# Performance work log

Measured on AMD Instinct MI355X. Metric: run time of the kernel, lower is better.

Reference implementation:

```python
import jax, jax.numpy as jnp
import numpy as np

H = 16  # num_heads
B, N, M, D = 4, 512, 2048, 1024
FF = 4096  # mlp_ratio * D
LN_EPS = 1e-5


def _ln(x, g, b):
    m = x.mean(-1, keepdims=True)
    v = ((x - m) ** 2).mean(-1, keepdims=True)
    return (x - m) * jax.lax.rsqrt(v + LN_EPS) * g + b


def _attn(q_in, k_in, v_in, wq, bq, wk, bk, wv, bv, wp, bp):
    b, n, d = q_in.shape
    m = k_in.shape[1]
    hd = d // H
    scale = hd ** -0.5
    q = (q_in @ wq + bq).reshape(b, n, H, hd) * scale
    k = (k_in @ wk + bk).reshape(b, m, H, hd)
    v = (v_in @ wv + bv).reshape(b, m, H, hd)
    attn = jax.nn.softmax(jnp.einsum('bnhd,bmhd->bhnm', q, k), axis=-1)
    out = jnp.einsum('bhnm,bmhd->bnhd', attn, v).reshape(b, n, d)
    return out @ wp + bp


def setup_inputs() -> dict:
    key = jax.random.key(0)
    ks = iter(jax.random.split(key, 32))
    rnd = lambda shape: jax.random.normal(next(ks), shape, dtype=jnp.float32)
    w = lambda *shape: rnd(shape) * 0.02
    inp = {
        'state': rnd((B, N, D)),
        'patches': rnd((B, M, D)),
        'patches_pos_embed': rnd((B, M, D)),
        'state_query': rnd((B, N, D)),
    }
    for p in ('ca', 'sa'):
        inp[f'{p}_wq'] = w(D, D); inp[f'{p}_bq'] = jnp.zeros((D,), jnp.float32)
        inp[f'{p}_wk'] = w(D, D); inp[f'{p}_bk'] = jnp.zeros((D,), jnp.float32)
        inp[f'{p}_wv'] = w(D, D); inp[f'{p}_bv'] = jnp.zeros((D,), jnp.float32)
        inp[f'{p}_wp'] = w(D, D); inp[f'{p}_bp'] = jnp.zeros((D,), jnp.float32)
    inp['w1'] = w(D, FF); inp['b1'] = jnp.zeros((FF,), jnp.float32)
    inp['w2'] = w(FF, D); inp['b2'] = jnp.zeros((D,), jnp.float32)
    for i in (1, 2, 3):
        inp[f'n{i}_g'] = jnp.ones((D,), jnp.float32)
        inp[f'n{i}_b'] = jnp.zeros((D,), jnp.float32)
        inp[f'ls{i}'] = jnp.full((D,), 1e-5, jnp.float32)
    return inp


def reference(state, patches, patches_pos_embed, state_query,
              ca_wq, ca_bq, ca_wk, ca_bk, ca_wv, ca_bv, ca_wp, ca_bp,
              sa_wq, sa_bq, sa_wk, sa_bk, sa_wv, sa_bv, sa_wp, sa_bp,
              w1, b1, w2, b2,
              n1_g, n1_b, n2_g, n2_b, n3_g, n3_b,
              ls1, ls2, ls3):
    # pre-norm path of TransformerLayer.forward_pre (dropouts/drop_path = 0)
    state = state + state_query
    kv = patches + patches_pos_embed
    cross = _attn(_ln(state, n1_g, n1_b), kv, patches,
                  ca_wq, ca_bq, ca_wk, ca_bk, ca_wv, ca_bv, ca_wp, ca_bp)
    state = state + cross * ls1
    ns = _ln(state, n2_g, n2_b)
    selfa = _attn(ns, ns, ns,
                  sa_wq, sa_bq, sa_wk, sa_bk, sa_wv, sa_bv, sa_wp, sa_bp)
    state = state + selfa * ls2
    h = jax.nn.gelu(_ln(state, n3_g, n3_b) @ w1 + b1)
    return state + (h @ w2 + b2) * ls3
```

## Files before the change

### kernel.cpp

```cpp
#include <hip/hip_runtime.h>

#define DEV __device__ __forceinline__

typedef __bf16 bf16x8 __attribute__((ext_vector_type(8)));
typedef float f32x4 __attribute__((ext_vector_type(4)));

DEV unsigned short f2bf(float f) {
  __bf16 h = (__bf16)f;
  return __builtin_bit_cast(unsigned short, h);
}
DEV unsigned int cvtpk(float lo, float hi) {
  unsigned int r;
  asm("v_cvt_pk_bf16_f32 %0, %1, %2" : "=v"(r) : "v"(lo), "v"(hi));
  return r;
}

DEV void gload16(const void* g, void* l) {
  __builtin_amdgcn_global_load_lds(
      (const __attribute__((address_space(1))) unsigned int*)g,
      (__attribute__((address_space(3))) unsigned int*)l, 16, 0, 0);
}

DEV void tconv_body(const float* __restrict__ W, unsigned short* __restrict__ Wt,
                    int K, int N, int bx, int by) {
  __shared__ float tile[32][33];
  const int tx = threadIdx.x, ty = threadIdx.y;
  const int n0 = bx * 32, k0 = by * 32;
#pragma unroll
  for (int i = 0; i < 32; i += 8)
    tile[ty + i][tx] = W[(size_t)(k0 + ty + i) * N + n0 + tx];
  __syncthreads();
#pragma unroll
  for (int i = 0; i < 32; i += 8)
    Wt[(size_t)(n0 + ty + i) * K + k0 + tx] = f2bf(tile[tx][ty + i]);
}

__global__ __launch_bounds__(256) void tconv_kernel(
    const float* __restrict__ W, unsigned short* __restrict__ Wt, int K, int N) {
  tconv_body(W, Wt, K, N, blockIdx.x, blockIdx.y);
}

struct TC8 { const float* src[8]; unsigned short* dst[8]; };
__global__ __launch_bounds__(256) void tconv8_kernel(TC8 p) {
  tconv_body(p.src[blockIdx.z], p.dst[blockIdx.z], 1024, 1024, blockIdx.x, blockIdx.y);
}

__global__ __launch_bounds__(256) void cat3_kernel(
    const float* __restrict__ a, const float* __restrict__ b,
    const float* __restrict__ c, float* __restrict__ o) {
  const int i = blockIdx.x * 256 + threadIdx.x;
  o[i] = i < 1024 ? a[i] : (i < 2048 ? b[i - 1024] : c[i - 2048]);
}

__global__ __launch_bounds__(256) void vtrans_kernel(
    const unsigned short* __restrict__ V, unsigned short* __restrict__ vT,
    int Nk, int RS, int colbase) {
  __shared__ unsigned short tile[32][33];
  const int tx = threadIdx.x, ty = threadIdx.y;
  const int k0 = blockIdx.x * 32;
  const int h = blockIdx.y >> 1, dt = (blockIdx.y & 1) * 32;
  const int b = blockIdx.z;
#pragma unroll
  for (int i = 0; i < 32; i += 8)
    tile[ty + i][tx] = V[(size_t)(b * Nk + k0 + ty + i) * RS + colbase + h * 64 + dt + tx];
  __syncthreads();
#pragma unroll
  for (int i = 0; i < 32; i += 8)
    vT[((size_t)(b * 16 + h) * 64 + dt + ty + i) * Nk + k0 + tx] = tile[tx][ty + i];
}

__global__ __launch_bounds__(256) void add_ln_kernel(
    const float* __restrict__ a, const float* b, float* x0_out,
    unsigned short* __restrict__ y, const float* __restrict__ gam,
    const float* __restrict__ bet) {
  const int row = blockIdx.x, t = threadIdx.x;
  const int c = t * 4;
  const size_t base = (size_t)row * 1024 + c;
  float4 v = *reinterpret_cast<const float4*>(a + base);
  if (b) {
    float4 v2 = *reinterpret_cast<const float4*>(b + base);
    v.x += v2.x; v.y += v2.y; v.z += v2.z; v.w += v2.w;
  }
  if (x0_out) *reinterpret_cast<float4*>(x0_out + base) = v;
  float s = v.x + v.y + v.z + v.w;
  float sq = v.x * v.x + v.y * v.y + v.z * v.z + v.w * v.w;
#pragma unroll
  for (int o = 32; o > 0; o >>= 1) {
    s += __shfl_xor(s, o);
    sq += __shfl_xor(sq, o);
  }
  __shared__ float ps[4], pq[4];
  const int w = t >> 6;
  if ((t & 63) == 0) { ps[w] = s; pq[w] = sq; }
  __syncthreads();
  s = ps[0] + ps[1] + ps[2] + ps[3];
  sq = pq[0] + pq[1] + pq[2] + pq[3];
  const float mean = s * (1.f / 1024.f);
  const float var = sq * (1.f / 1024.f) - mean * mean;
  const float rstd = rsqrtf(var + 1e-5f);
  float4 gv = *reinterpret_cast<const float4*>(gam + c);
  float4 bv = *reinterpret_cast<const float4*>(bet + c);
  uint2 o2;
  o2.x = cvtpk((v.x - mean) * rstd * gv.x + bv.x, (v.y - mean) * rstd * gv.y + bv.y);
  o2.y = cvtpk((v.z - mean) * rstd * gv.z + bv.z, (v.w - mean) * rstd * gv.w + bv.w);
  *reinterpret_cast<uint2*>(y + base) = o2;
}

__global__ __launch_bounds__(256) void kvcast_kernel(
    const float* __restrict__ p, const float* __restrict__ pe,
    unsigned short* __restrict__ kvo, unsigned short* __restrict__ po) {
  const size_t i = ((size_t)blockIdx.x * 256 + threadIdx.x) * 4;
  float4 a = *reinterpret_cast<const float4*>(p + i);
  float4 b = *reinterpret_cast<const float4*>(pe + i);
  uint2 kv2, p2;
  kv2.x = cvtpk(a.x + b.x, a.y + b.y);
  kv2.y = cvtpk(a.z + b.z, a.w + b.w);
  p2.x = cvtpk(a.x, a.y);
  p2.y = cvtpk(a.z, a.w);
  *reinterpret_cast<uint2*>(kvo + i) = kv2;
  *reinterpret_cast<uint2*>(po + i) = p2;
}

DEV void xcd_swizzle(int gx, int gy, int& bx, int& by, int& bz) {
  const int gxy = gx * gy;
  const int nwg = gxy * gridDim.z;
  const int orig = (blockIdx.z * gy + blockIdx.y) * gx + blockIdx.x;
  const int q = nwg >> 3, r = nwg & 7;
  const int xcd = orig & 7;
  int wgid = (xcd < r ? xcd * (q + 1) : r * (q + 1) + (xcd - r) * q) + (orig >> 3);
  bz = wgid / gxy;
  wgid -= bz * gxy;
  if (gy >= gx) { by = wgid / gx; bx = wgid - by * gx; }
  else          { bx = wgid / gy; by = wgid - bx * gy; }
}

template <int BM, int BN>
DEV void gemm_core(const unsigned short* __restrict__ A,
                   const unsigned short* __restrict__ Bt,
                   unsigned short* As, unsigned short* Bs,
                   int brow, int bcol, int K, int lda, int koff,
                   f32x4 (&acc)[BM / 32][BN / 32]) {
  constexpr int WM = BM / 32, WN = BN / 32;
  const int t = threadIdx.x;
  const int lane = t & 63, w = t >> 6;
  const int wr = w >> 1, wc = w & 1;
  const int g = lane >> 4, lr = lane & 15;
  const int srow = lane >> 2, scol = (lane & 3) * 8;

  auto stage = [&](int buf, int k0) {
#pragma unroll
    for (int i = 0; i < BM / 64; i++) {
      const int r0 = (i * 4 + w) * 16;
      gload16(A + (size_t)(brow + r0 + srow) * lda + koff + k0 + scol,
              &As[buf * BM * 32 + r0 * 32]);
    }
#pragma unroll
    for (int i = 0; i < BN / 64; i++) {
      const int r0 = (i * 4 + w) * 16;
      gload16(Bt + (size_t)(bcol + r0 + srow) * lda + koff + k0 + scol,
              &Bs[buf * BN * 32 + r0 * 32]);
    }
  };

  stage(0, 0);
  const int nk = K / 32;
  int cur = 0;
  for (int kt = 0; kt < nk; kt++) {
    __syncthreads();
    if (kt + 1 < nk) stage(cur ^ 1, (kt + 1) * 32);
    bf16x8 af[WM], bfr[WN];
#pragma unroll
    for (int m = 0; m < WM; m++)
      af[m] = *reinterpret_cast<const bf16x8*>(
          &As[cur * BM * 32 + (wr * (BM / 2) + m * 16 + lr) * 32 + g * 8]);
#pragma unroll
    for (int n = 0; n < WN; n++)
      bfr[n] = *reinterpret_cast<const bf16x8*>(
          &Bs[cur * BN * 32 + (wc * (BN / 2) + n * 16 + lr) * 32 + g * 8]);
#pragma unroll
    for (int m = 0; m < WM; m++)
#pragma unroll
      for (int n = 0; n < WN; n++)
        acc[m][n] = __builtin_amdgcn_mfma_f32_16x16x32_bf16(af[m], bfr[n], acc[m][n], 0, 0, 0);
    cur ^= 1;
  }
}

template <int EPI, int BM, int BN>
__global__ __launch_bounds__(256) void gemm_kernel(
    const unsigned short* __restrict__ A, const unsigned short* __restrict__ Bt,
    const float* __restrict__ bias, const float* resid,
    const float* __restrict__ ls, void* outp, int M, int N, int K, int lda) {
  constexpr int WM = BM / 32;
  constexpr int WN = BN / 32;
  __shared__ __align__(16) unsigned short As[2 * BM * 32];
  __shared__ __align__(16) unsigned short Bs[2 * BN * 32];
  const int t = threadIdx.x;
  const int lane = t & 63, w = t >> 6;
  const int wr = w >> 1, wc = w & 1;
  const int g = lane >> 4, lr = lane & 15;

  int bx, by, bz;
  xcd_swizzle(gridDim.x, gridDim.y, bx, by, bz);
  const int brow = by * BM, bcol = bx * BN;

  f32x4 acc[WM][WN] = {};
  gemm_core<BM, BN>(A, Bt, As, Bs, brow, bcol, K, lda, bz * K, acc);

#pragma unroll
  for (int m = 0; m < WM; m++) {
    const int row0 = brow + wr * (BM / 2) + m * 16 + g * 4;
#pragma unroll
    for (int n = 0; n < WN; n++) {
      const int col = bcol + wc * (BN / 2) + n * 16 + lr;
      const float bv = (EPI == 4) ? 0.f : bias[col];
#pragma unroll
      for (int r = 0; r < 4; r++) {
        const float v = acc[m][n][r] + bv;
        const size_t idx = (size_t)(row0 + r) * N + col;
        if (EPI == 0) {
          ((unsigned short*)outp)[idx] = f2bf(v);
        } else if (EPI == 2) {
          ((float*)outp)[idx] = resid[idx] + v * ls[col];
        } else if (EPI == 3) {
          const float tth = tanhf(0.7978845608028654f * (v + 0.044715f * v * v * v));
          ((unsigned short*)outp)[idx] = f2bf(0.5f * v * (1.f + tth));
        } else {
          ((float*)outp)[(size_t)bz * M * N + idx] = v;
        }
      }
    }
  }
}

struct G3 {
  const unsigned short* A[3]; const unsigned short* Bt[3];
  const float* bias[3]; unsigned short* out[3]; int ecum[3];
};
__global__ __launch_bounds__(256) void gemm3_kernel(G3 p, int N, int K) {
  constexpr int BM = 128, BN = 128, WM = BM / 32, WN = BN / 32;
  __shared__ __align__(16) unsigned short As[2 * BM * 32];
  __shared__ __align__(16) unsigned short Bs[2 * BN * 32];
  const int t = threadIdx.x;
  const int lane = t & 63, w = t >> 6;
  const int wr = w >> 1, wc = w & 1;
  const int g = lane >> 4, lr = lane & 15;

  int bx, by, bz;
  xcd_swizzle(gridDim.x, gridDim.y, bx, by, bz);
  const int s = (by >= p.ecum[0]) + (by >= p.ecum[1]);
  const int byloc = by - (s ? p.ecum[s - 1] : 0);
  const unsigned short* A = p.A[s];
  const unsigned short* Bt = p.Bt[s];
  const float* bias = p.bias[s];
  unsigned short* outp = p.out[s];
  const int brow = byloc * BM, bcol = bx * BN;

  f32x4 acc[WM][WN] = {};
  gemm_core<BM, BN>(A, Bt, As, Bs, brow, bcol, K, K, 0, acc);

#pragma unroll
  for (int m = 0; m < WM; m++) {
    const int row0 = brow + wr * (BM / 2) + m * 16 + g * 4;
#pragma unroll
    for (int n = 0; n < WN; n++) {
      const int col = bcol + wc * (BN / 2) + n * 16 + lr;
      const float bv = bias[col];
#pragma unroll
      for (int r = 0; r < 4; r++)
        outp[(size_t)(row0 + r) * N + col] = f2bf(acc[m][n][r] + bv);
    }
  }
}

__global__ __launch_bounds__(256) void splitk_red_kernel(
    const float* __restrict__ p, const float* __restrict__ bias,
    const float* __restrict__ resid, const float* __restrict__ ls,
    float* __restrict__ out) {
  const size_t i = ((size_t)blockIdx.x * 256 + threadIdx.x) * 4;
  const int c = (int)(i & 1023);
  float4 a = *reinterpret_cast<const float4*>(p + i);
  float4 b = *reinterpret_cast<const float4*>(p + 2048ull * 1024 + i);
  float4 rv = *reinterpret_cast<const float4*>(resid + i);
  float4 bb = *reinterpret_cast<const float4*>(bias + c);
  float4 lv = *reinterpret_cast<const float4*>(ls + c);
  float4 o;
  o.x = rv.x + (a.x + b.x + bb.x) * lv.x;
  o.y = rv.y + (a.y + b.y + bb.y) * lv.y;
  o.z = rv.z + (a.z + b.z + bb.z) * lv.z;
  o.w = rv.w + (a.w + b.w + bb.w) * lv.w;
  *reinterpret_cast<float4*>(out + i) = o;
}

__global__ __launch_bounds__(512) void attn_kernel(
    const unsigned short* __restrict__ Q, const unsigned short* __restrict__ Kp,
    const unsigned short* __restrict__ vT, unsigned short* __restrict__ O,
    int RSq, int RSk, int Nq, int Nk, float k2) {
  __shared__ __align__(16) unsigned short Ks[2][128 * 72];
  __shared__ __align__(16) unsigned short Vs[2][64 * 136];
  __shared__ __align__(16) unsigned short Ps[128 * 136];
  const int t = threadIdx.x, lane = t & 63, w = t >> 6;
  const int qt = blockIdx.y, h = blockIdx.x & 15, b = blockIdx.x >> 4;
  const int g = lane >> 4, lr = lane & 15;
  const int ksrow = t >> 2, kscol = (t & 3) * 16;
  const int vsrow = t >> 3, vscol = (t & 7) * 16;

  uint4 qr[2];
  {
    const unsigned short* qp = Q + (size_t)(b * Nq + qt * 128 + w * 16 + lr) * RSq + h * 64 + g * 8;
    qr[0] = *reinterpret_cast<const uint4*>(qp);
    qr[1] = *reinterpret_cast<const uint4*>(qp + 32);
  }
  float m_i = -1e30f, l_i = 0.f;
  f32x4 acc_o[4] = {};

  auto kaddr = [&](int kv0) {
    return reinterpret_cast<const uint4*>(
        Kp + (size_t)(b * Nk + kv0 + ksrow) * RSk + h * 64 + kscol);
  };
  auto vaddr = [&](int kv0) {
    return reinterpret_cast<const uint4*>(
        vT + ((size_t)(b * 16 + h) * 64 + vsrow) * Nk + kv0 + vscol);
  };

  uint4 kr0 = kaddr(0)[0], kr1 = kaddr(0)[1];
  uint4 vr0 = vaddr(0)[0], vr1 = vaddr(0)[1];

  int cur = 0;
  for (int kv0 = 0; kv0 < Nk; kv0 += 128) {
    *reinterpret_cast<uint4*>(&Ks[cur][ksrow * 72 + kscol]) = kr0;
    *reinterpret_cast<uint4*>(&Ks[cur][ksrow * 72 + kscol + 8]) = kr1;
    *reinterpret_cast<uint4*>(&Vs[cur][vsrow * 136 + vscol]) = vr0;
    *reinterpret_cast<uint4*>(&Vs[cur][vsrow * 136 + vscol + 8]) = vr1;
    __syncthreads();
    if (kv0 + 128 < Nk) {
      kr0 = kaddr(kv0 + 128)[0]; kr1 = kaddr(kv0 + 128)[1];
      vr0 = vaddr(kv0 + 128)[0]; vr1 = vaddr(kv0 + 128)[1];
    }

    f32x4 accs[8] = {};
    __builtin_amdgcn_s_setprio(1);
#pragma unroll
    for (int d0 = 0; d0 < 64; d0 += 32) {
      bf16x8 qf = __builtin_bit_cast(bf16x8, qr[d0 >> 5]);
#pragma unroll
      for (int m = 0; m < 8; m++) {
        bf16x8 kf = *reinterpret_cast<const bf16x8*>(&Ks[cur][(m * 16 + lr) * 72 + d0 + g * 8]);
        accs[m] = __builtin_amdgcn_mfma_f32_16x16x32_bf16(kf, qf, accs[m], 0, 0, 0);
      }
    }
    __builtin_amdgcn_s_setprio(0);
    float pmax = -1e30f;
#pragma unroll
    for (int m = 0; m < 8; m++)
#pragma unroll
      for (int r = 0; r < 4; r++) pmax = fmaxf(pmax, accs[m][r]);
    pmax = fmaxf(pmax, __shfl_xor(pmax, 16));
    pmax = fmaxf(pmax, __shfl_xor(pmax, 32));
    const float pm2 = pmax * k2;
    if (!__all(pm2 <= m_i + 8.f)) {
      const float m_new = fmaxf(m_i, pm2);
      const float corr = exp2f(m_i - m_new);
      m_i = m_new;
      l_i *= corr;
#pragma unroll
      for (int r = 0; r < 4; r++) {
        const float cf = __shfl(corr, g * 4 + r);
#pragma unroll
        for (int n = 0; n < 4; n++) acc_o[n][r] *= cf;
      }
    }
    float psum = 0.f;
#pragma unroll
    for (int m = 0; m < 8; m++) {
      float p0 = exp2f(fmaf(accs[m][0], k2, -m_i));
      float p1 = exp2f(fmaf(accs[m][1], k2, -m_i));
      float p2 = exp2f(fmaf(accs[m][2], k2, -m_i));
      float p3 = exp2f(fmaf(accs[m][3], k2, -m_i));
      psum += p0 + p1 + p2 + p3;
      uint2 pk;
      pk.x = cvtpk(p0, p1);
      pk.y = cvtpk(p2, p3);
      *reinterpret_cast<uint2*>(&Ps[(w * 16 + lr) * 136 + m * 16 + g * 4]) = pk;
    }
    psum += __shfl_xor(psum, 16);
    psum += __shfl_xor(psum, 32);
    l_i += psum;
    __builtin_amdgcn_s_setprio(1);
#pragma unroll
    for (int ks = 0; ks < 4; ks++) {
      bf16x8 pf = *reinterpret_cast<const bf16x8*>(&Ps[(w * 16 + lr) * 136 + ks * 32 + g * 8]);
#pragma unroll
      for (int n = 0; n < 4; n++) {
        bf16x8 vf = *reinterpret_cast<const bf16x8*>(&Vs[cur][(n * 16 + lr) * 136 + ks * 32 + g * 8]);
        acc_o[n] = __builtin_amdgcn_mfma_f32_16x16x32_bf16(pf, vf, acc_o[n], 0, 0, 0);
      }
    }
    __builtin_amdgcn_s_setprio(0);
    cur ^= 1;
  }
#pragma unroll
  for (int r = 0; r < 4; r++) {
    const float li = __shfl(l_i, g * 4 + r);
    const float inv = 1.f / li;
    const int qrow = qt * 128 + w * 16 + g * 4 + r;
#pragma unroll
    for (int n = 0; n < 4; n++)
      O[(size_t)(b * Nq + qrow) * 1024 + h * 64 + n * 16 + lr] = f2bf(acc_o[n][r] * inv);
  }
}

extern "C" void kernel_launch(void* const* d_in, const int* in_sizes, int n_in,
                              void* d_out, int out_size, void* d_ws, size_t ws_size,
                              hipStream_t stream) {
  const float* state = (const float*)d_in[0];
  const float* patches = (const float*)d_in[1];
  const float* ppe = (const float*)d_in[2];
  const float* squery = (const float*)d_in[3];
  const float* ca_wq = (const float*)d_in[4];
  const float* ca_bq = (const float*)d_in[5];
  const float* ca_wk = (const float*)d_in[6];
  const float* ca_bk = (const float*)d_in[7];
  const float* ca_wv = (const float*)d_in[8];
  const float* ca_bv = (const float*)d_in[9];
  const float* ca_wp = (const float*)d_in[10];
  const float* ca_bp = (const float*)d_in[11];
  const float* sa_wq = (const float*)d_in[12];
  const float* sa_bq = (const float*)d_in[13];
  const float* sa_wk = (const float*)d_in[14];
  const float* sa_bk = (const float*)d_in[15];
  const float* sa_wv = (const float*)d_in[16];
  const float* sa_bv = (const float*)d_in[17];
  const float* sa_wp = (const float*)d_in[18];
  const float* sa_bp = (const float*)d_in[19];
  const float* w1 = (const float*)d_in[20];
  const float* b1 = (const float*)d_in[21];
  const float* w2 = (const float*)d_in[22];
  const float* b2 = (const float*)d_in[23];
  const float* n1_g = (const float*)d_in[24];
  const float* n1_b = (const float*)d_in[25];
  const float* ls1 = (const float*)d_in[26];
  const float* n2_g = (const float*)d_in[27];
  const float* n2_b = (const float*)d_in[28];
  const float* ls2 = (const float*)d_in[29];
  const float* n3_g = (const float*)d_in[30];
  const float* n3_b = (const float*)d_in[31];
  const float* ls3 = (const float*)d_in[32];

  char* wsp = (char*)d_ws;
  auto alloc = [&](size_t bytes) {
    void* p = (void*)wsp;
    wsp += (bytes + 255) & ~(size_t)255;
    return p;
  };
  float* stateF = (float*)alloc(2048ull * 1024 * 4);
  unsigned short* lnB = (unsigned short*)alloc(2048ull * 1024 * 2);
  unsigned short* kvB = (unsigned short*)alloc(8192ull * 1024 * 2);
  unsigned short* patB = (unsigned short*)alloc(8192ull * 1024 * 2);
  unsigned short* qB = (unsigned short*)alloc(2048ull * 1024 * 2);
  unsigned short* kB = (unsigned short*)alloc(8192ull * 1024 * 2);
  unsigned short* vB = (unsigned short*)alloc(8192ull * 1024 * 2);
  unsigned short* oB = (unsigned short*)alloc(2048ull * 1024 * 2);
  unsigned short* hB = kvB;
  unsigned short* qkvB = kB;
  unsigned short* vTc = patB;
  unsigned short* vTs = qB;
  float* mlp2p = (float*)patB;
  unsigned short* ca_wqt = (unsigned short*)alloc(1024ull * 1024 * 2);
  unsigned short* ca_wkt = (unsigned short*)alloc(1024ull * 1024 * 2);
  unsigned short* ca_wvt = (unsigned short*)alloc(1024ull * 1024 * 2);
  unsigned short* ca_wpt = (unsigned short*)alloc(1024ull * 1024 * 2);
  unsigned short* sa_wqkvt = (unsigned short*)alloc(3072ull * 1024 * 2);
  unsigned short* sa_wpt = (unsigned short*)alloc(1024ull * 1024 * 2);
  unsigned short* w1t = (unsigned short*)alloc(4096ull * 1024 * 2);
  unsigned short* w2t = (unsigned short*)alloc(4096ull * 1024 * 2);
  float* sa_bqkv = (float*)alloc(3072 * 4);

  const dim3 tb(32, 8);
  TC8 tc;
  tc.src[0] = ca_wq; tc.dst[0] = ca_wqt;
  tc.src[1] = ca_wk; tc.dst[1] = ca_wkt;
  tc.src[2] = ca_wv; tc.dst[2] = ca_wvt;
  tc.src[3] = ca_wp; tc.dst[3] = ca_wpt;
  tc.src[4] = sa_wq; tc.dst[4] = sa_wqkvt;
  tc.src[5] = sa_wk; tc.dst[5] = sa_wqkvt + 1024ull * 1024;
  tc.src[6] = sa_wv; tc.dst[6] = sa_wqkvt + 2048ull * 1024;
  tc.src[7] = sa_wp; tc.dst[7] = sa_wpt;
  tconv8_kernel<<<dim3(32, 32, 8), tb, 0, stream>>>(tc);
  tconv_kernel<<<dim3(128, 32), tb, 0, stream>>>(w1, w1t, 1024, 4096);
  tconv_kernel<<<dim3(32, 128), tb, 0, stream>>>(w2, w2t, 4096, 1024);
  cat3_kernel<<<12, 256, 0, stream>>>(sa_bq, sa_bk, sa_bv, sa_bqkv);

  add_ln_kernel<<<2048, 256, 0, stream>>>(state, squery, stateF, lnB, n1_g, n1_b);
  kvcast_kernel<<<8192, 256, 0, stream>>>(patches, ppe, kvB, patB);

  const float k2 = 0.125f * 1.4426950408889634f;

  G3 g3;
  g3.A[0] = lnB;  g3.Bt[0] = ca_wqt; g3.bias[0] = ca_bq; g3.out[0] = qB;  g3.ecum[0] = 16;
  g3.A[1] = kvB;  g3.Bt[1] = ca_wkt; g3.bias[1] = ca_bk; g3.out[1] = kB;  g3.ecum[1] = 80;
  g3.A[2] = patB; g3.Bt[2] = ca_wvt; g3.bias[2] = ca_bv; g3.out[2] = vB;  g3.ecum[2] = 144;
  gemm3_kernel<<<dim3(8, 144), 256, 0, stream>>>(g3, 1024, 1024);
  vtrans_kernel<<<dim3(64, 32, 4), tb, 0, stream>>>(vB, vTc, 2048, 1024, 0);
  attn_kernel<<<dim3(64, 4), 512, 0, stream>>>(qB, kB, vTc, oB, 1024, 1024, 512, 2048, k2);
  gemm_kernel<2, 64, 64><<<dim3(16, 32), 256, 0, stream>>>(oB, ca_wpt, ca_bp, stateF, ls1, stateF, 2048, 1024, 1024, 1024);

  add_ln_kernel<<<2048, 256, 0, stream>>>(stateF, nullptr, nullptr, lnB, n2_g, n2_b);
  gemm_kernel<0, 128, 64><<<dim3(48, 16), 256, 0, stream>>>(lnB, sa_wqkvt, sa_bqkv, nullptr, nullptr, qkvB, 2048, 3072, 1024, 1024);
  vtrans_kernel<<<dim3(16, 32, 4), tb, 0, stream>>>(qkvB, vTs, 512, 3072, 2048);
  attn_kernel<<<dim3(64, 4), 512, 0, stream>>>(qkvB, qkvB + 1024, vTs, oB, 3072, 3072, 512, 512, k2);
  gemm_kernel<2, 64, 64><<<dim3(16, 32), 256, 0, stream>>>(oB, sa_wpt, sa_bp, stateF, ls2, stateF, 2048, 1024, 1024, 1024);

  add_ln_kernel<<<2048, 256, 0, stream>>>(stateF, nullptr, nullptr, lnB, n3_g, n3_b);
  gemm_kernel<3, 128, 128><<<dim3(32, 16), 256, 0, stream>>>(lnB, w1t, b1, nullptr, nullptr, hB, 2048, 4096, 1024, 1024);
  gemm_kernel<4, 128, 64><<<dim3(16, 16, 2), 256, 0, stream>>>(hB, w2t, nullptr, nullptr, nullptr, mlp2p, 2048, 1024, 2048, 4096);
  splitk_red_kernel<<<2048, 256, 0, stream>>>(mlp2p, b2, stateF, ls3, (float*)d_out);
}
```

Measured before the change: 314.7 us.

## Fuse prelude kernels into one launch and write V transposed from GEMM epilogues

Merges the weight transpose/cast, kv cast, first add+LayerNorm and bias concat into a single prelude kernel launch. The V-projection GEMMs (cross and self attention) now write V directly in transposed per-head layout through an LDS-staged epilogue, removing both vtrans kernels and an intermediate V buffer round trip. It also raises wave priority around the MFMA block in the GEMM inner loop. In exchange the GEMMs need larger shared memory for the transpose staging, which may lower occupancy, and the prelude mixes heterogeneous work in one grid.

```diff
diff --git a/kernel.cpp b/kernel.cpp
--- a/kernel.cpp
+++ b/kernel.cpp
@@ -24,7 +24,8 @@
 DEV void tconv_body(const float* __restrict__ W, unsigned short* __restrict__ Wt,
                     int K, int N, int bx, int by) {
   __shared__ float tile[32][33];
-  const int tx = threadIdx.x, ty = threadIdx.y;
+  const int t = threadIdx.x;
+  const int tx = t & 31, ty = t >> 5;
   const int n0 = bx * 32, k0 = by * 32;
 #pragma unroll
   for (int i = 0; i < 32; i += 8)
@@ -35,45 +36,10 @@
     Wt[(size_t)(n0 + ty + i) * K + k0 + tx] = f2bf(tile[tx][ty + i]);
 }
 
-__global__ __launch_bounds__(256) void tconv_kernel(
-    const float* __restrict__ W, unsigned short* __restrict__ Wt, int K, int N) {
-  tconv_body(W, Wt, K, N, blockIdx.x, blockIdx.y);
-}
-
-struct TC8 { const float* src[8]; unsigned short* dst[8]; };
-__global__ __launch_bounds__(256) void tconv8_kernel(TC8 p) {
-  tconv_body(p.src[blockIdx.z], p.dst[blockIdx.z], 1024, 1024, blockIdx.x, blockIdx.y);
-}
-
-__global__ __launch_bounds__(256) void cat3_kernel(
-    const float* __restrict__ a, const float* __restrict__ b,
-    const float* __restrict__ c, float* __restrict__ o) {
-  const int i = blockIdx.x * 256 + threadIdx.x;
-  o[i] = i < 1024 ? a[i] : (i < 2048 ? b[i - 1024] : c[i - 2048]);
-}
-
-__global__ __launch_bounds__(256) void vtrans_kernel(
-    const unsigned short* __restrict__ V, unsigned short* __restrict__ vT,
-    int Nk, int RS, int colbase) {
-  __shared__ unsigned short tile[32][33];
-  const int tx = threadIdx.x, ty = threadIdx.y;
-  const int k0 = blockIdx.x * 32;
-  const int h = blockIdx.y >> 1, dt = (blockIdx.y & 1) * 32;
-  const int b = blockIdx.z;
-#pragma unroll
-  for (int i = 0; i < 32; i += 8)
-    tile[ty + i][tx] = V[(size_t)(b * Nk + k0 + ty + i) * RS + colbase + h * 64 + dt + tx];
-  __syncthreads();
-#pragma unroll
-  for (int i = 0; i < 32; i += 8)
-    vT[((size_t)(b * 16 + h) * 64 + dt + ty + i) * Nk + k0 + tx] = tile[tx][ty + i];
-}
-
-__global__ __launch_bounds__(256) void add_ln_kernel(
-    const float* __restrict__ a, const float* b, float* x0_out,
-    unsigned short* __restrict__ y, const float* __restrict__ gam,
-    const float* __restrict__ bet) {
-  const int row = blockIdx.x, t = threadIdx.x;
+DEV void add_ln_body(const float* __restrict__ a, const float* b, float* x0_out,
+                     unsigned short* __restrict__ y, const float* __restrict__ gam,
+                     const float* __restrict__ bet, int row) {
+  const int t = threadIdx.x;
   const int c = t * 4;
   const size_t base = (size_t)row * 1024 + c;
   float4 v = *reinterpret_cast<const float4*>(a + base);
@@ -106,10 +72,10 @@
   *reinterpret_cast<uint2*>(y + base) = o2;
 }
 
-__global__ __launch_bounds__(256) void kvcast_kernel(
-    const float* __restrict__ p, const float* __restrict__ pe,
-    unsigned short* __restrict__ kvo, unsigned short* __restrict__ po) {
-  const size_t i = ((size_t)blockIdx.x * 256 + threadIdx.x) * 4;
+DEV void kvcast_body(const float* __restrict__ p, const float* __restrict__ pe,
+                     unsigned short* __restrict__ kvo, unsigned short* __restrict__ po,
+                     int bid) {
+  const size_t i = ((size_t)bid * 256 + threadIdx.x) * 4;
   float4 a = *reinterpret_cast<const float4*>(p + i);
   float4 b = *reinterpret_cast<const float4*>(pe + i);
   uint2 kv2, p2;
@@ -119,6 +85,44 @@
   p2.y = cvtpk(a.z, a.w);
   *reinterpret_cast<uint2*>(kvo + i) = kv2;
   *reinterpret_cast<uint2*>(po + i) = p2;
+}
+
+struct Pre {
+  const float* sqw[8]; unsigned short* sqd[8];
+  const float* w1; unsigned short* w1t;
+  const float* w2; unsigned short* w2t;
+  const float* state; const float* squery; float* stateF; unsigned short* lnB;
+  const float* n1_g; const float* n1_b;
+  const float* patches; const float* ppe; unsigned short* kvB; unsigned short* patB;
+  const float* bq; const float* bk; const float* bv; float* bqkv;
+};
+__global__ __launch_bounds__(256) void prelude_kernel(Pre p) {
+  const int bid = blockIdx.x;
+  if (bid < 8192) {
+    kvcast_body(p.patches, p.ppe, p.kvB, p.patB, bid);
+  } else if (bid < 16384) {
+    const int i = bid - 8192;
+    const int m = i >> 10, wi = i & 1023;
+    tconv_body(p.sqw[m], p.sqd[m], 1024, 1024, wi & 31, wi >> 5);
+  } else if (bid < 20480) {
+    const int i = bid - 16384;
+    tconv_body(p.w1, p.w1t, 1024, 4096, i & 127, i >> 7);
+  } else if (bid < 24576) {
+    const int i = bid - 20480;
+    tconv_body(p.w2, p.w2t, 4096, 1024, i & 31, i >> 5);
+  } else if (bid < 26624) {
+    add_ln_body(p.state, p.squery, p.stateF, p.lnB, p.n1_g, p.n1_b, bid - 24576);
+  } else {
+    const int i = (bid - 26624) * 256 + threadIdx.x;
+    p.bqkv[i] = i < 1024 ? p.bq[i] : (i < 2048 ? p.bk[i - 1024] : p.bv[i - 2048]);
+  }
+}
+
+__global__ __launch_bounds__(256) void add_ln_kernel(
+    const float* __restrict__ a, const float* b, float* x0_out,
+    unsigned short* __restrict__ y, const float* __restrict__ gam,
+    const float* __restrict__ bet) {
+  add_ln_body(a, b, x0_out, y, gam, bet, blockIdx.x);
 }
 
 DEV void xcd_swizzle(int gx, int gy, int& bx, int& by, int& bz) {
@@ -177,12 +181,54 @@
     for (int n = 0; n < WN; n++)
       bfr[n] = *reinterpret_cast<const bf16x8*>(
           &Bs[cur * BN * 32 + (wc * (BN / 2) + n * 16 + lr) * 32 + g * 8]);
+    __builtin_amdgcn_s_setprio(1);
 #pragma unroll
     for (int m = 0; m < WM; m++)
 #pragma unroll
       for (int n = 0; n < WN; n++)
         acc[m][n] = __builtin_amdgcn_mfma_f32_16x16x32_bf16(af[m], bfr[n], acc[m][n], 0, 0, 0);
+    __builtin_amdgcn_s_setprio(0);
     cur ^= 1;
+  }
+}
+
+template <int BM, int BN>
+DEV void epilogue_vT(f32x4 (&acc)[BM / 32][BN / 32], unsigned short* smem,
+                     unsigned short* __restrict__ vT, const float* __restrict__ bias,
+                     int brow, int bcol, int vcol0, int vNk, int rpb) {
+  constexpr int WM = BM / 32, WN = BN / 32;
+  constexpr int LDT = 136;
+  const int t = threadIdx.x, lane = t & 63, w = t >> 6;
+  const int wr = w >> 1, wc = w & 1;
+  const int g = lane >> 4, lr = lane & 15;
+  __syncthreads();
+#pragma unroll
+  for (int m = 0; m < WM; m++) {
+    const int row0 = wr * (BM / 2) + m * 16 + g * 4;
+#pragma unroll
+    for (int n = 0; n < WN; n++) {
+      const int cc = wc * (BN / 2) + n * 16 + lr;
+      const float bv = bias[bcol + cc];
+      uint2 pk;
+      pk.x = cvtpk(acc[m][n][0] + bv, acc[m][n][1] + bv);
+      pk.y = cvtpk(acc[m][n][2] + bv, acc[m][n][3] + bv);
+      *reinterpret_cast<uint2*>(&smem[cc * LDT + row0]) = pk;
+    }
+  }
+  __syncthreads();
+  const int b = brow / rpb;
+  const int kvb = brow % rpb;
+  constexpr int ITERS = BM * BN / (256 * 8);
+#pragma unroll
+  for (int it = 0; it < ITERS; it++) {
+    const int idx = it * 256 + t;
+    const int cc = idx / (BM / 8);
+    const int ch = idx % (BM / 8);
+    const int dg = bcol + cc - vcol0;
+    const int h = dg >> 6, d = dg & 63;
+    uint4 v = *reinterpret_cast<uint4*>(&smem[cc * LDT + ch * 8]);
+    *reinterpret_cast<uint4*>(
+        &vT[((size_t)(b * 16 + h) * 64 + d) * vNk + kvb + ch * 8]) = v;
   }
 }
 
@@ -190,11 +236,16 @@
 __global__ __launch_bounds__(256) void gemm_kernel(
     const unsigned short* __restrict__ A, const unsigned short* __restrict__ Bt,
     const float* __restrict__ bias, const float* resid,
-    const float* __restrict__ ls, void* outp, int M, int N, int K, int lda) {
+    const float* __restrict__ ls, void* outp, int M, int N, int K, int lda,
+    unsigned short* vT, int vcol0, int vNk, int rpb) {
   constexpr int WM = BM / 32;
   constexpr int WN = BN / 32;
-  __shared__ __align__(16) unsigned short As[2 * BM * 32];
-  __shared__ __align__(16) unsigned short Bs[2 * BN * 32];
+  constexpr int STG = 2 * BM * 32 + 2 * BN * 32;
+  constexpr int TRN = BN * 136;
+  constexpr int SME = (EPI == 5 && TRN > STG) ? TRN : STG;
+  __shared__ __align__(16) unsigned short smem[SME];
+  unsigned short* As = smem;
+  unsigned short* Bs = smem + 2 * BM * 32;
   const int t = threadIdx.x;
   const int lane = t & 63, w = t >> 6;
   const int wr = w >> 1, wc = w & 1;
@@ -207,6 +258,11 @@
   f32x4 acc[WM][WN] = {};
   gemm_core<BM, BN>(A, Bt, As, Bs, brow, bcol, K, lda, bz * K, acc);
 
+  if (EPI == 5 && bcol >= vcol0) {
+    epilogue_vT<BM, BN>(acc, smem, vT, bias, brow, bcol, vcol0, vNk, rpb);
+    return;
+  }
+
 #pragma unroll
   for (int m = 0; m < WM; m++) {
     const int row0 = brow + wr * (BM / 2) + m * 16 + g * 4;
@@ -218,7 +274,7 @@
       for (int r = 0; r < 4; r++) {
         const float v = acc[m][n][r] + bv;
         const size_t idx = (size_t)(row0 + r) * N + col;
-        if (EPI == 0) {
+        if (EPI == 0 || EPI == 5) {
           ((unsigned short*)outp)[idx] = f2bf(v);
         } else if (EPI == 2) {
           ((float*)outp)[idx] = resid[idx] + v * ls[col];
@@ -236,11 +292,16 @@
 struct G3 {
   const unsigned short* A[3]; const unsigned short* Bt[3];
   const float* bias[3]; unsigned short* out[3]; int ecum[3];
+  unsigned short* vT; int vNk; int rpb;
 };
 __global__ __launch_bounds__(256) void gemm3_kernel(G3 p, int N, int K) {
   constexpr int BM = 128, BN = 128, WM = BM / 32, WN = BN / 32;
-  __shared__ __align__(16) unsigned short As[2 * BM * 32];
-  __shared__ __align__(16) unsigned short Bs[2 * BN * 32];
+  constexpr int STG = 2 * BM * 32 + 2 * BN * 32;
+  constexpr int TRN = BN * 136;
+  constexpr int SME = (TRN > STG) ? TRN : STG;
+  __shared__ __align__(16) unsigned short smem[SME];
+  unsigned short* As = smem;
+  unsigned short* Bs = smem + 2 * BM * 32;
   const int t = threadIdx.x;
   const int lane = t & 63, w = t >> 6;
   const int wr = w >> 1, wc = w & 1;
@@ -253,12 +314,16 @@
   const unsigned short* A = p.A[s];
   const unsigned short* Bt = p.Bt[s];
   const float* bias = p.bias[s];
-  unsigned short* outp = p.out[s];
   const int brow = byloc * BM, bcol = bx * BN;
 
   f32x4 acc[WM][WN] = {};
   gemm_core<BM, BN>(A, Bt, As, Bs, brow, bcol, K, K, 0, acc);
 
+  if (s == 2) {
+    epilogue_vT<BM, BN>(acc, smem, p.vT, bias, brow, bcol, 0, p.vNk, p.rpb);
+    return;
+  }
+  unsigned short* outp = p.out[s];
 #pragma unroll
   for (int m = 0; m < WM; m++) {
     const int row0 = brow + wr * (BM / 2) + m * 16 + g * 4;
@@ -463,7 +528,7 @@
   unsigned short* oB = (unsigned short*)alloc(2048ull * 1024 * 2);
   unsigned short* hB = kvB;
   unsigned short* qkvB = kB;
-  unsigned short* vTc = patB;
+  unsigned short* vTc = vB;
   unsigned short* vTs = qB;
   float* mlp2p = (float*)patB;
   unsigned short* ca_wqt = (unsigned short*)alloc(1024ull * 1024 * 2);
@@ -476,43 +541,40 @@
   unsigned short* w2t = (unsigned short*)alloc(4096ull * 1024 * 2);
   float* sa_bqkv = (float*)alloc(3072 * 4);
 
-  const dim3 tb(32, 8);
-  TC8 tc;
-  tc.src[0] = ca_wq; tc.dst[0] = ca_wqt;
-  tc.src[1] = ca_wk; tc.dst[1] = ca_wkt;
-  tc.src[2] = ca_wv; tc.dst[2] = ca_wvt;
-  tc.src[3] = ca_wp; tc.dst[3] = ca_wpt;
-  tc.src[4] = sa_wq; tc.dst[4] = sa_wqkvt;
-  tc.src[5] = sa_wk; tc.dst[5] = sa_wqkvt + 1024ull * 1024;
-  tc.src[6] = sa_wv; tc.dst[6] = sa_wqkvt + 2048ull * 1024;
-  tc.src[7] = sa_wp; tc.dst[7] = sa_wpt;
-  tconv8_kernel<<<dim3(32, 32, 8), tb, 0, stream>>>(tc);
-  tconv_kernel<<<dim3(128, 32), tb, 0, stream>>>(w1, w1t, 1024, 4096);
-  tconv_kernel<<<dim3(32, 128), tb, 0, stream>>>(w2, w2t, 4096, 1024);
-  cat3_kernel<<<12, 256, 0, stream>>>(sa_bq, sa_bk, sa_bv, sa_bqkv);
-
-  add_ln_kernel<<<2048, 256, 0, stream>>>(state, squery, stateF, lnB, n1_g, n1_b);
-  kvcast_kernel<<<8192, 256, 0, stream>>>(patches, ppe, kvB, patB);
+  Pre pre;
+  pre.sqw[0] = ca_wq; pre.sqd[0] = ca_wqt;
+  pre.sqw[1] = ca_wk; pre.sqd[1] = ca_wkt;
+  pre.sqw[2] = ca_wv; pre.sqd[2] = ca_wvt;
+  pre.sqw[3] = ca_wp; pre.sqd[3] = ca_wpt;
+  pre.sqw[4] = sa_wq; pre.sqd[4] = sa_wqkvt;
+  pre.sqw[5] = sa_wk; pre.sqd[5] = sa_wqkvt + 1024ull * 1024;
+  pre.sqw[6] = sa_wv; pre.sqd[6] = sa_wqkvt + 2048ull * 1024;
+  pre.sqw[7] = sa_wp; pre.sqd[7] = sa_wpt;
+  pre.w1 = w1; pre.w1t = w1t; pre.w2 = w2; pre.w2t = w2t;
+  pre.state = state; pre.squery = squery; pre.stateF = stateF; pre.lnB = lnB;
+  pre.n1_g = n1_g; pre.n1_b = n1_b;
+  pre.patches = patches; pre.ppe = ppe; pre.kvB = kvB; pre.patB = patB;
+  pre.bq = sa_bq; pre.bk = sa_bk; pre.bv = sa_bv; pre.bqkv = sa_bqkv;
+  prelude_kernel<<<26636, 256, 0, stream>>>(pre);
 
   const float k2 = 0.125f * 1.4426950408889634f;
 
   G3 g3;
-  g3.A[0] = lnB;  g3.Bt[0] = ca_wqt; g3.bias[0] = ca_bq; g3.out[0] = qB;  g3.ecum[0] = 16;
-  g3.A[1] = kvB;  g3.Bt[1] = ca_wkt; g3.bias[1] = ca_bk; g3.out[1] = kB;  g3.ecum[1] = 80;
-  g3.A[2] = patB; g3.Bt[2] = ca_wvt; g3.bias[2] = ca_bv; g3.out[2] = vB;  g3.ecum[2] = 144;
+  g3.A[0] = lnB;  g3.Bt[0] = ca_wqt; g3.bias[0] = ca_bq; g3.out[0] = qB;      g3.ecum[0] = 16;
+  g3.A[1] = kvB;  g3.Bt[1] = ca_wkt; g3.bias[1] = ca_bk; g3.out[1] = kB;      g3.ecum[1] = 80;
+  g3.A[2] = patB; g3.Bt[2] = ca_wvt; g3.bias[2] = ca_bv; g3.out[2] = nullptr; g3.ecum[2] = 144;
+  g3.vT = vTc; g3.vNk = 2048; g3.rpb = 2048;
   gemm3_kernel<<<dim3(8, 144), 256, 0, stream>>>(g3, 1024, 1024);
-  vtrans_kernel<<<dim3(64, 32, 4), tb, 0, stream>>>(vB, vTc, 2048, 1024, 0);
   attn_kernel<<<dim3(64, 4), 512, 0, stream>>>(qB, kB, vTc, oB, 1024, 1024, 512, 2048, k2);
-  gemm_kernel<2, 64, 64><<<dim3(16, 32), 256, 0, stream>>>(oB, ca_wpt, ca_bp, stateF, ls1, stateF, 2048, 1024, 1024, 1024);
+  gemm_kernel<2, 64, 64><<<dim3(16, 32), 256, 0, stream>>>(oB, ca_wpt, ca_bp, stateF, ls1, stateF, 2048, 1024, 1024, 1024, nullptr, 0, 0, 0);
 
   add_ln_kernel<<<2048, 256, 0, stream>>>(stateF, nullptr, nullptr, lnB, n2_g, n2_b);
-  gemm_kernel<0, 128, 64><<<dim3(48, 16), 256, 0, stream>>>(lnB, sa_wqkvt, sa_bqkv, nullptr, nullptr, qkvB, 2048, 3072, 1024, 1024);
-  vtrans_kernel<<<dim3(16, 32, 4), tb, 0, stream>>>(qkvB, vTs, 512, 3072, 2048);
+  gemm_kernel<5, 128, 64><<<dim3(48, 16), 256, 0, stream>>>(lnB, sa_wqkvt, sa_bqkv, nullptr, nullptr, qkvB, 2048, 3072, 1024, 1024, vTs, 2048, 512, 512);
   attn_kernel<<<dim3(64, 4), 512, 0, stream>>>(qkvB, qkvB + 1024, vTs, oB, 3072, 3072, 512, 512, k2);
-  gemm_kernel<2, 64, 64><<<dim3(16, 32), 256, 0, stream>>>(oB, sa_wpt, sa_bp, stateF, ls2, stateF, 2048, 1024, 1024, 1024);
+  gemm_kernel<2, 64, 64><<<dim3(16, 32), 256, 0, stream>>>(oB, sa_wpt, sa_bp, stateF, ls2, stateF, 2048, 1024, 1024, 1024, nullptr, 0, 0, 0);
 
   add_ln_kernel<<<2048, 256, 0, stream>>>(stateF, nullptr, nullptr, lnB, n3_g, n3_b);
-  gemm_kernel<3, 128, 128><<<dim3(32, 16), 256, 0, stream>>>(lnB, w1t, b1, nullptr, nullptr, hB, 2048, 4096, 1024, 1024);
-  gemm_kernel<4, 128, 64><<<dim3(16, 16, 2), 256, 0, stream>>>(hB, w2t, nullptr, nullptr, nullptr, mlp2p, 2048, 1024, 2048, 4096);
+  gemm_kernel<3, 128, 128><<<dim3(32, 16), 256, 0, stream>>>(lnB, w1t, b1, nullptr, nullptr, hB, 2048, 4096, 1024, 1024, nullptr, 0, 0, 0);
+  gemm_kernel<4, 128, 64><<<dim3(16, 16, 2), 256, 0, stream>>>(hB, w2t, nullptr, nullptr, nullptr, mlp2p, 2048, 1024, 2048, 4096, nullptr, 0, 0, 0);
   splitk_red_kernel<<<2048, 256, 0, stream>>>(mlp2p, b2, stateF, ls3, (float*)d_out);
 }
```

Result: faster. 284.5 us (-9.6%).
